# Optimization experiments

Hardware: AMD Instinct MI355X
Metric: run time of the kernel (lower is better)

## Reference

```python
import jax, jax.numpy as jnp
import numpy as np

EPS = 1e-5
CHUNK = 256
N_LAYERS = 4
D_MODEL = 1024
D_INNER = 2048
D_HEAD = 64
N_HEADS = 32
D_STATE = 64
D_CONV = 4
CONV_DIM = D_INNER + 2 * D_STATE  # ngroups=1
D_IN_PROJ = 2 * D_INNER + 2 * D_STATE + N_HEADS


def silu(x):
    return x * jax.nn.sigmoid(x)


def rmsnorm(x, w):
    return x * jax.lax.rsqrt(jnp.mean(x * x, axis=-1, keepdims=True) + EPS) * w


def segsum(x):
    # x: [..., T] -> [..., T, T] lower-triangular segment sums, -inf above diag
    T = x.shape[-1]
    cs = jnp.cumsum(x, axis=-1)
    ss = cs[..., :, None] - cs[..., None, :]
    mask = jnp.tril(jnp.ones((T, T), dtype=bool))
    return jnp.where(mask, ss, -jnp.inf)


def ssd(X, A, B, C, chunk):
    # X: [b,l,h,p] (already scaled by dt), A: [b,l,h] (= dt * A_head), B,C: [b,l,n] (ngroups=1)
    b, l, h, p = X.shape
    c = l // chunk
    X = X.reshape(b, c, chunk, h, p)
    A = A.reshape(b, c, chunk, h).transpose(0, 3, 1, 2)  # [b,h,c,l]
    B = B.reshape(b, c, chunk, -1)
    C = C.reshape(b, c, chunk, -1)
    Acs = jnp.cumsum(A, axis=-1)  # [b,h,c,l]
    # intra-chunk (diagonal blocks)
    Lm = jnp.exp(segsum(A))  # [b,h,c,l,l]
    Y_diag = jnp.einsum('bcln,bcsn,bhcls,bcshp->bclhp', C, B, Lm, X)
    # chunk end states
    decay_states = jnp.exp(Acs[..., -1:] - Acs)  # [b,h,c,l]
    states = jnp.einsum('bcln,bhcl,bclhp->bchpn', B, decay_states, X)
    # inter-chunk recurrence (c is small -> dense segsum over chunks)
    A_last = jnp.pad(Acs[..., -1], ((0, 0), (0, 0), (1, 0)))  # [b,h,c+1]
    decay_chunk = jnp.exp(segsum(A_last))  # [b,h,c+1,c+1]
    states = jnp.concatenate([jnp.zeros_like(states[:, :1]), states], axis=1)
    new_states = jnp.einsum('bhzc,bchpn->bzhpn', decay_chunk, states)
    states = new_states[:, :-1]  # state entering each chunk
    Y_off = jnp.einsum('bcln,bchpn,bhcl->bclhp', C, states, jnp.exp(Acs))
    return (Y_diag + Y_off).reshape(b, l, h, p)


def mamba2_layer(x, in_w, conv_w, conv_b, dt_bias, A_log, D, gnorm_w, out_w):
    b, l, _ = x.shape
    zxbcdt = jnp.einsum('bld,ed->ble', x, in_w)  # [b,l,D_IN_PROJ]
    z = zxbcdt[..., :D_INNER]
    xBC = zxbcdt[..., D_INNER:D_INNER + CONV_DIM]
    dt = zxbcdt[..., D_INNER + CONV_DIM:]  # [b,l,h]
    # depthwise causal conv1d + silu
    xpad = jnp.pad(xBC, ((0, 0), (D_CONV - 1, 0), (0, 0)))
    xconv = conv_b
    for k in range(D_CONV):
        xconv = xconv + xpad[:, k:k + l, :] * conv_w[:, k]
    xBC = silu(xconv)
    x_in = xBC[..., :D_INNER]
    B = xBC[..., D_INNER:D_INNER + D_STATE]
    C = xBC[..., D_INNER + D_STATE:]
    dt = jax.nn.softplus(dt + dt_bias)  # [b,l,h]
    A = -jnp.exp(A_log)  # [h]
    X = x_in.reshape(b, l, N_HEADS, D_HEAD)
    y = ssd(X * dt[..., None], dt * A, B, C, CHUNK)
    y = y + D[None, None, :, None] * X
    y = y.reshape(b, l, D_INNER)
    y = rmsnorm(y * silu(z), gnorm_w)
    return jnp.einsum('ble,de->bld', y, out_w)


def setup_inputs() -> dict:
    key = jax.random.key(0)
    ks = jax.random.split(key, 8)
    x = jax.random.normal(ks[0], (2, 2048, D_MODEL), dtype=jnp.float32)
    in_proj_w = jax.random.normal(ks[1], (N_LAYERS, D_IN_PROJ, D_MODEL), dtype=jnp.float32) * 0.02
    conv_w = jax.random.uniform(ks[2], (N_LAYERS, CONV_DIM, D_CONV), dtype=jnp.float32, minval=-0.5, maxval=0.5)
    conv_b = jnp.zeros((N_LAYERS, CONV_DIM), dtype=jnp.float32)
    A_log = jnp.log(jax.random.uniform(ks[3], (N_LAYERS, N_HEADS), dtype=jnp.float32, minval=1.0, maxval=16.0))
    dt0 = jax.random.uniform(ks[4], (N_LAYERS, N_HEADS), dtype=jnp.float32, minval=0.001, maxval=0.1)
    dt_bias = dt0 + jnp.log(-jnp.expm1(-dt0))  # inverse softplus
    D = jnp.ones((N_LAYERS, N_HEADS), dtype=jnp.float32)
    gnorm_w = jnp.ones((N_LAYERS, D_INNER), dtype=jnp.float32)
    out_proj_w = jax.random.normal(ks[5], (N_LAYERS, D_MODEL, D_INNER), dtype=jnp.float32) * 0.02
    rms_w = jnp.ones((N_LAYERS, D_MODEL), dtype=jnp.float32)
    return {"x": x, "in_proj_w": in_proj_w, "conv_w": conv_w, "conv_b": conv_b,
            "dt_bias": dt_bias, "A_log": A_log, "D": D, "gnorm_w": gnorm_w,
            "out_proj_w": out_proj_w, "rms_w": rms_w}


def reference(x, in_proj_w, conv_w, conv_b, dt_bias, A_log, D, gnorm_w, out_proj_w, rms_w):
    for i in range(N_LAYERS):
        x = x + mamba2_layer(rmsnorm(x, rms_w[i]), in_proj_w[i], conv_w[i], conv_b[i],
                             dt_bias[i], A_log[i], D[i], gnorm_w[i], out_proj_w[i])
    return x
```

## Files before the change

kernel.cpp:

```cpp
#include <hip/hip_runtime.h>
#include <cmath>

#define BATCH 2
#define LSEQ 2048
#define DMODEL 1024
#define DINNER 2048
#define NHEADS 32
#define DHEAD 64
#define DSTATE 64
#define DCONV 4
#define CONVDIM (DINNER + 2*DSTATE)
#define DINPROJ (2*DINNER + 2*DSTATE + NHEADS)
#define DINPROJ_PAD 4352
#define CHUNKSZ 256
#define NCHUNK (LSEQ/CHUNKSZ)
#define MROWS (BATCH*LSEQ)
#define EPSF 1e-5f

typedef __attribute__((ext_vector_type(8))) short shortx8;
typedef __attribute__((ext_vector_type(4))) short shortx4;
typedef __attribute__((ext_vector_type(4))) float floatx4;

__device__ __forceinline__ ushort f2bf(float f) {
  unsigned u = __float_as_uint(f);
  unsigned r = (u + 0x7fffu + ((u >> 16) & 1u)) >> 16;
  return (ushort)r;
}
__device__ __forceinline__ float bf2f(ushort b) {
  return __uint_as_float(((unsigned)b) << 16);
}

__device__ __forceinline__ shortx8 pack8(float4 a, float4 b) {
  shortx8 r;
  r[0] = (short)f2bf(a.x); r[1] = (short)f2bf(a.y);
  r[2] = (short)f2bf(a.z); r[3] = (short)f2bf(a.w);
  r[4] = (short)f2bf(b.x); r[5] = (short)f2bf(b.y);
  r[6] = (short)f2bf(b.z); r[7] = (short)f2bf(b.w);
  return r;
}

__device__ __forceinline__ void async_load16(const void* g, void* l) {
  __builtin_amdgcn_global_load_lds(
      (const __attribute__((address_space(1))) void*)g,
      (__attribute__((address_space(3))) void*)l, 16, 0, 0);
}

__device__ __forceinline__ float block_reduce_sum_256(float v, float* sb) {
  for (int off = 32; off > 0; off >>= 1) v += __shfl_down(v, off, 64);
  int lane = threadIdx.x & 63, wid = threadIdx.x >> 6;
  if (lane == 0) sb[wid] = v;
  __syncthreads();
  return sb[0] + sb[1] + sb[2] + sb[3];
}

__global__ __launch_bounds__(256) void cvt_bf16_k(const float* __restrict__ src,
                                                  ushort* __restrict__ dst,
                                                  size_t n_src, size_t n_dst) {
  size_t i = (size_t)blockIdx.x * 256 + threadIdx.x;
  if (i >= n_dst) return;
  float v = (i < n_src) ? src[i] : 0.f;
  dst[i] = f2bf(v);
}

__global__ __launch_bounds__(256) void cvt_w_all(const float* __restrict__ in_w,
                                                 const float* __restrict__ out_w,
                                                 ushort* __restrict__ in_bf,
                                                 ushort* __restrict__ out_bf) {
  unsigned g = (blockIdx.x * 256u + threadIdx.x) * 8u;
  const unsigned PL = (unsigned)DINPROJ_PAD * DMODEL;
  const unsigned n1 = 4u * PL;
  const unsigned n2 = 4u * DMODEL * DINNER;
  if (g < n1) {
    unsigned layer = g / PL, rem = g % PL;
    unsigned row = rem / DMODEL, col = rem % DMODEL;
    shortx8 o;
    if (row < DINPROJ) {
      const float* sp = in_w + ((size_t)layer * DINPROJ + row) * DMODEL + col;
      float4 a = *(const float4*)sp;
      float4 b = *(const float4*)(sp + 4);
      o = pack8(a, b);
    } else {
#pragma unroll
      for (int j = 0; j < 8; j++) o[j] = 0;
    }
    *(shortx8*)(in_bf + g) = o;
  } else if (g < n1 + n2) {
    unsigned j = g - n1;
    const float* sp = out_w + j;
    float4 a = *(const float4*)sp;
    float4 b = *(const float4*)(sp + 4);
    *(shortx8*)(out_bf + j) = pack8(a, b);
  }
}

__global__ __launch_bounds__(256) void rmsnorm_k(const float* __restrict__ x,
                                                 const float* __restrict__ w,
                                                 ushort* __restrict__ out) {
  __shared__ float sb[4];
  int r = blockIdx.x;
  const float* xr = x + (size_t)r * DMODEL;
  ushort* orow = out + (size_t)r * DMODEL;
  int c0 = threadIdx.x * 4;
  float4 v4 = *(const float4*)(xr + c0);
  float ssq = v4.x * v4.x + v4.y * v4.y + v4.z * v4.z + v4.w * v4.w;
  float s = block_reduce_sum_256(ssq, sb);
  float sc = rsqrtf(s / (float)DMODEL + EPSF);
  float4 w4 = *(const float4*)(w + c0);
  shortx4 o;
  o[0] = (short)f2bf(v4.x * sc * w4.x);
  o[1] = (short)f2bf(v4.y * sc * w4.y);
  o[2] = (short)f2bf(v4.z * sc * w4.z);
  o[3] = (short)f2bf(v4.w * sc * w4.w);
  *(shortx4*)(orow + c0) = o;
}

__device__ __forceinline__ void stage_tile(const ushort* __restrict__ A,
                                           const ushort* __restrict__ B,
                                           char* lb, int m0, int n0, int K, int k0,
                                           int wid, int rA, int sA) {
#pragma unroll
  for (int rd = 0; rd < 2; rd++) {
    int r = rd * 64 + rA;
    int sl = sA ^ ((r ^ (r >> 2)) & 3);
    async_load16(A + (size_t)(m0 + r) * K + (k0 + sl * 8), lb + rd * 4096 + wid * 1024);
  }
#pragma unroll
  for (int rd = 0; rd < 2; rd++) {
    int r = rd * 64 + rA;
    int sl = sA ^ ((r ^ (r >> 2)) & 3);
    async_load16(B + (size_t)(n0 + r) * K + (k0 + sl * 8), lb + 8192 + rd * 4096 + wid * 1024);
  }
}

__global__ __launch_bounds__(256, 3) void gemm_nt_mfma_pipe(
    const ushort* __restrict__ A, const ushort* __restrict__ B,
    ushort* __restrict__ Cbf, int M, int N, int K,
    int nbx, int rw, int rh) {
  __shared__ __align__(16) char lds[3][16384];
  int tid = threadIdx.x;
  int wid = tid >> 6, lane = tid & 63;
  int quad = lane >> 4, lrow = lane & 15;

  int d = blockIdx.x;
  int xcd = d & 7, wi = d >> 3;
  int ra = nbx / rw;
  int rn = xcd % ra, rm = xcd / ra;
  int bx = rn * rw + wi % rw;
  int by = rm * rh + wi / rw;

  int m0 = by * 128, n0 = bx * 128;
  int wm = (wid >> 1) * 64, wn = (wid & 1) * 64;
  int rA = tid >> 2, sA = tid & 3;

  floatx4 acc[4][4];
#pragma unroll
  for (int i = 0; i < 4; i++)
#pragma unroll
    for (int j = 0; j < 4; j++) acc[i][j] = (floatx4){0.f, 0.f, 0.f, 0.f};

  int NT = K >> 5;
#pragma unroll
  for (int t = 0; t < 2; t++)
    stage_tile(A, B, lds[t], m0, n0, K, t * 32, wid, rA, sA);

  int cur = 0, sb = 2;
  for (int t = 0; t < NT; t++) {
    if (t < NT - 1) asm volatile("s_waitcnt vmcnt(4)" ::: "memory");
    else            asm volatile("s_waitcnt vmcnt(0)" ::: "memory");
    __builtin_amdgcn_s_barrier();
    __builtin_amdgcn_sched_barrier(0);
    if (t + 2 < NT) {
      stage_tile(A, B, lds[sb], m0, n0, K, (t + 2) * 32, wid, rA, sA);
      sb = (sb == 2) ? 0 : sb + 1;
    }

    const char* Ab = lds[cur];
    const char* Bb = Ab + 8192;
    cur = (cur == 2) ? 0 : cur + 1;
    shortx8 af[4], bfr[4];
#pragma unroll
    for (int i = 0; i < 4; i++) {
      int r = wm + i * 16 + lrow;
      af[i] = *(const shortx8*)(Ab + r * 64 + ((quad ^ ((r ^ (r >> 2)) & 3)) << 4));
    }
#pragma unroll
    for (int j = 0; j < 4; j++) {
      int r = wn + j * 16 + lrow;
      bfr[j] = *(const shortx8*)(Bb + r * 64 + ((quad ^ ((r ^ (r >> 2)) & 3)) << 4));
    }
    __builtin_amdgcn_s_setprio(1);
#pragma unroll
    for (int i = 0; i < 4; i++)
#pragma unroll
      for (int j = 0; j < 4; j++)
        acc[i][j] = __builtin_amdgcn_mfma_f32_16x16x32_bf16(af[i], bfr[j], acc[i][j], 0, 0, 0);
    __builtin_amdgcn_s_setprio(0);
  }

#pragma unroll
  for (int i = 0; i < 4; i++) {
    int r0 = m0 + wm + i * 16 + quad * 4;
#pragma unroll
    for (int j = 0; j < 4; j++) {
      int n = n0 + wn + j * 16 + lrow;
      if (n < N)
#pragma unroll
        for (int r = 0; r < 4; r++)
          Cbf[(size_t)(r0 + r) * N + n] = f2bf(acc[i][j][r]);
    }
  }
}

__device__ __forceinline__ void stage_tile64(const ushort* __restrict__ A,
                                             const ushort* __restrict__ B,
                                             char* lb, int m0, int n0, int K, int k0,
                                             int wid, int rA, int sA) {
#pragma unroll
  for (int rd = 0; rd < 2; rd++) {
    int r = rd * 64 + rA;
    int sl = sA ^ ((r ^ (r >> 2)) & 3);
    async_load16(A + (size_t)(m0 + r) * K + (k0 + sl * 8), lb + rd * 4096 + wid * 1024);
  }
  {
    int r = rA;
    int sl = sA ^ ((r ^ (r >> 2)) & 3);
    async_load16(B + (size_t)(n0 + r) * K + (k0 + sl * 8), lb + 8192 + wid * 1024);
  }
}

__global__ __launch_bounds__(256, 2) void gemm_nt_64(
    const ushort* __restrict__ A, const ushort* __restrict__ B,
    float* __restrict__ C, const float* __restrict__ resid,
    int M, int N, int K, int nbx, int rw, int rh) {
  __shared__ __align__(16) char lds[3][12288];
  int tid = threadIdx.x;
  int wid = tid >> 6, lane = tid & 63;
  int quad = lane >> 4, lrow = lane & 15;

  int d = blockIdx.x;
  int xcd = d & 7, wi = d >> 3;
  int ra = nbx / rw;
  int rn = xcd % ra, rm = xcd / ra;
  int bx = rn * rw + wi % rw;
  int by = rm * rh + wi / rw;

  int m0 = by * 128, n0 = bx * 64;
  int wm = (wid >> 1) * 64, wn = (wid & 1) * 32;
  int rA = tid >> 2, sA = tid & 3;

  floatx4 acc[4][2];
#pragma unroll
  for (int i = 0; i < 4; i++)
#pragma unroll
    for (int j = 0; j < 2; j++) acc[i][j] = (floatx4){0.f, 0.f, 0.f, 0.f};

  int NT = K >> 5;
#pragma unroll
  for (int t = 0; t < 2; t++)
    stage_tile64(A, B, lds[t], m0, n0, K, t * 32, wid, rA, sA);

  int cur = 0, sb = 2;
  for (int t = 0; t < NT; t++) {
    if (t < NT - 1) asm volatile("s_waitcnt vmcnt(3)" ::: "memory");
    else            asm volatile("s_waitcnt vmcnt(0)" ::: "memory");
    __builtin_amdgcn_s_barrier();
    __builtin_amdgcn_sched_barrier(0);
    if (t + 2 < NT) {
      stage_tile64(A, B, lds[sb], m0, n0, K, (t + 2) * 32, wid, rA, sA);
      sb = (sb == 2) ? 0 : sb + 1;
    }

    const char* Ab = lds[cur];
    const char* Bb = Ab + 8192;
    cur = (cur == 2) ? 0 : cur + 1;
    shortx8 af[4], bfr[2];
#pragma unroll
    for (int i = 0; i < 4; i++) {
      int r = wm + i * 16 + lrow;
      af[i] = *(const shortx8*)(Ab + r * 64 + ((quad ^ ((r ^ (r >> 2)) & 3)) << 4));
    }
#pragma unroll
    for (int j = 0; j < 2; j++) {
      int r = wn + j * 16 + lrow;
      bfr[j] = *(const shortx8*)(Bb + r * 64 + ((quad ^ ((r ^ (r >> 2)) & 3)) << 4));
    }
    __builtin_amdgcn_s_setprio(1);
#pragma unroll
    for (int i = 0; i < 4; i++)
#pragma unroll
      for (int j = 0; j < 2; j++)
        acc[i][j] = __builtin_amdgcn_mfma_f32_16x16x32_bf16(af[i], bfr[j], acc[i][j], 0, 0, 0);
    __builtin_amdgcn_s_setprio(0);
  }

  bool hasR = (resid != nullptr);
#pragma unroll
  for (int i = 0; i < 4; i++) {
    int r0 = m0 + wm + i * 16 + quad * 4;
#pragma unroll
    for (int j = 0; j < 2; j++) {
      int n = n0 + wn + j * 16 + lrow;
#pragma unroll
      for (int r = 0; r < 4; r++) {
        size_t idx = (size_t)(r0 + r) * N + n;
        float v = acc[i][j][r];
        if (hasR) v += resid[idx];
        C[idx] = v;
      }
    }
  }
}

__global__ __launch_bounds__(256) void convcum_k(const ushort* __restrict__ zxbf,
                                                 const float* __restrict__ cw,
                                                 const float* __restrict__ cb,
                                                 ushort* __restrict__ xbf,
                                                 const float* __restrict__ dt_bias,
                                                 const float* __restrict__ A_log,
                                                 float* __restrict__ dt_sp,
                                                 float* __restrict__ dtA_cs) {
  __shared__ float buf[256];
  int tid = threadIdx.x;
  if (blockIdx.x < MROWS / 8) {
    int r0 = blockIdx.x * 8;
    int bstart = r0 & ~(LSEQ - 1);
#pragma unroll
    for (int rep = 0; rep < 2; rep++) {
      int ch;
      if (rep == 0) ch = tid * 8;
      else { if (tid >= (CONVDIM - 2048) / 8) break; ch = 2048 + tid * 8; }
      float wv[8][4], bias[8];
#pragma unroll
      for (int j = 0; j < 8; j++) {
        float4 w4 = *(const float4*)(cw + (ch + j) * 4);
        wv[j][0] = w4.x; wv[j][1] = w4.y; wv[j][2] = w4.z; wv[j][3] = w4.w;
        bias[j] = cb[ch + j];
      }
      float xw[11][8];
#pragma unroll
      for (int wr = 0; wr < 11; wr++) {
        int rr = r0 - 3 + wr;
        if (rr < bstart) {
#pragma unroll
          for (int j = 0; j < 8; j++) xw[wr][j] = 0.f;
        } else {
          shortx8 v = *(const shortx8*)(zxbf + (size_t)rr * DINPROJ + DINNER + ch);
#pragma unroll
          for (int j = 0; j < 8; j++) xw[wr][j] = bf2f((ushort)v[j]);
        }
      }
#pragma unroll
      for (int o = 0; o < 8; o++) {
        shortx8 ov;
#pragma unroll
        for (int j = 0; j < 8; j++) {
          float acc = bias[j];
#pragma unroll
          for (int k = 0; k < 4; k++) acc += xw[o + k][j] * wv[j][k];
          float s = acc / (1.f + expf(-acc));
          ov[j] = (short)f2bf(s);
        }
        *(shortx8*)(xbf + (size_t)(r0 + o) * CONVDIM + ch) = ov;
      }
    }
  } else {
    int bid = blockIdx.x - MROWS / 8;
    int h = bid & 31, c = (bid >> 5) & 7, b = bid >> 8;
    int l = tid;
    float Aneg = -expf(A_log[h]);
    int row = b * LSEQ + c * CHUNKSZ + l;
    float v = bf2f(zxbf[(size_t)row * DINPROJ + DINNER + CONVDIM + h]) + dt_bias[h];
    float dtv = (v > 20.f) ? v : log1pf(expf(v));
    dt_sp[row * 32 + h] = dtv;
    buf[l] = dtv * Aneg;
    __syncthreads();
    for (int off = 1; off < 256; off <<= 1) {
      float add = (l >= off) ? buf[l - off] : 0.f;
      __syncthreads();
      buf[l] += add;
      __syncthreads();
    }
    dtA_cs[(size_t)bid * CHUNKSZ + l] = buf[l];
  }
}

#define ST_STRIDE 72
__global__ __launch_bounds__(256) void states_mfma(const ushort* __restrict__ xbf,
                                                   const float* __restrict__ dt_sp,
                                                   const float* __restrict__ dtA_cs,
                                                   float* __restrict__ st_raw) {
  __shared__ ushort XT[64 * ST_STRIDE];
  __shared__ ushort BT[64 * ST_STRIDE];
  __shared__ float wrow[64];
  int bid = blockIdx.x;
  int h = bid & 31, c = (bid >> 5) & 7, b = bid >> 8;
  int tid = threadIdx.x;
  int w = tid >> 6, lane = tid & 63;
  int quad = lane >> 4, lrow = lane & 15;
  int cbase = bid * CHUNKSZ;
  int rowbase = b * LSEQ + c * CHUNKSZ;
  float T = dtA_cs[cbase + CHUNKSZ - 1];
  floatx4 acc[4];
  for (int jt = 0; jt < 4; jt++) acc[jt] = (floatx4){0.f, 0.f, 0.f, 0.f};
  int half = tid & 31, srb = tid >> 5;
  int ekey = (half & 7) << 3;
  for (int lt = 0; lt < 4; lt++) {
    __syncthreads();
    if (tid < 64) {
      int row = rowbase + lt * 64 + tid;
      wrow[tid] = dt_sp[row * 32 + h] * __expf(T - dtA_cs[cbase + lt * 64 + tid]);
    }
    __syncthreads();
    for (int pass = 0; pass < 8; pass++) {
      int sr = srb + pass * 8;
      int row = rowbase + lt * 64 + sr;
      uint bv = *(const uint*)(xbf + (size_t)row * CONVDIM + DINNER + 2 * half);
      uint xv = *(const uint*)(xbf + (size_t)row * CONVDIM + h * DHEAD + 2 * half);
      float wv = wrow[sr];
      int sc = sr ^ ekey;
      BT[(2 * half) * ST_STRIDE + sc]     = (ushort)(bv & 0xffff);
      BT[(2 * half + 1) * ST_STRIDE + sc] = (ushort)(bv >> 16);
      XT[(2 * half) * ST_STRIDE + sc]     = f2bf(bf2f((ushort)(xv & 0xffff)) * wv);
      XT[(2 * half + 1) * ST_STRIDE + sc] = f2bf(bf2f((ushort)(xv >> 16)) * wv);
    }
    __syncthreads();
    int arow = w * 16 + lrow;
    int akey = ((arow >> 1) & 7) << 3;
    for (int kk = 0; kk < 64; kk += 32) {
      shortx8 af = *(const shortx8*)&XT[arow * ST_STRIDE + ((kk + quad * 8) ^ akey)];
      for (int jt = 0; jt < 4; jt++) {
        int brow = jt * 16 + lrow;
        int bkey = ((brow >> 1) & 7) << 3;
        shortx8 bf = *(const shortx8*)&BT[brow * ST_STRIDE + ((kk + quad * 8) ^ bkey)];
        acc[jt] = __builtin_amdgcn_mfma_f32_16x16x32_bf16(af, bf, acc[jt], 0, 0, 0);
      }
    }
  }
  size_t base = (size_t)bid * (DHEAD * DSTATE);
  for (int jt = 0; jt < 4; jt++) {
    int n = jt * 16 + lrow;
    for (int r = 0; r < 4; r++) {
      int p = w * 16 + quad * 4 + r;
      st_raw[base + (size_t)p * 64 + n] = acc[jt][r];
    }
  }
}

__global__ __launch_bounds__(256) void scan_k(float* __restrict__ st,
                                              const float* __restrict__ dtA_cs) {
  int bid = blockIdx.x;
  int seg = bid & 3, h = (bid >> 2) & 31, b = bid >> 7;
  int tid = threadIdx.x;
  int off = seg * 1024;
  float s[4];
  for (int i = 0; i < 4; i++) s[i] = 0.f;
  for (int c = 0; c < NCHUNK; c++) {
    int g = (b * NCHUNK + c) * 32 + h;
    float dec = expf(dtA_cs[(size_t)g * CHUNKSZ + CHUNKSZ - 1]);
    size_t base = (size_t)g * (DHEAD * DSTATE) + off;
    for (int i = 0; i < 4; i++) {
      int idx = tid + i * 256;
      float raw = st[base + idx];
      st[base + idx] = s[i];
      s[i] = s[i] * dec + raw;
    }
  }
}

#define BS_STRIDE 72
#define XT_STRIDE 68
#define PW_STRIDE 72
__global__ __launch_bounds__(256) void ydiag_mfma(const ushort* __restrict__ xbf,
                                                  const float* __restrict__ dt_sp,
                                                  const float* __restrict__ dtA_cs,
                                                  const float* __restrict__ st_in,
                                                  ushort* __restrict__ Y) {
  __shared__ ushort Bs[64 * BS_STRIDE];
  __shared__ ushort XsT[64 * XT_STRIDE];
  __shared__ ushort Pw[4 * 16 * PW_STRIDE];
  __shared__ float cs[256];
  int tid = threadIdx.x;
  int w = tid >> 6, lane = tid & 63;
  int quad = lane >> 4, lrow = lane & 15;
  int bid = blockIdx.x;
  int lt = bid & 3, h = (bid >> 2) & 31, c = (bid >> 7) & 7, b = bid >> 10;
  int g = (b * NCHUNK + c) * 32 + h;
  int cbase = g * CHUNKSZ;
  int rowbase = b * LSEQ + c * CHUNKSZ;

  cs[tid] = dtA_cs[cbase + tid];
  __syncthreads();

  int mrow = lt * 64 + w * 16;
  float csl[4];
  for (int r = 0; r < 4; r++) csl[r] = cs[mrow + quad * 4 + r];

  shortx8 Cf[2];
  {
    const ushort* cp = xbf + (size_t)(rowbase + mrow + lrow) * CONVDIM + DINNER + DSTATE;
    for (int q = 0; q < 2; q++)
      Cf[q] = *(const shortx8*)(cp + q * 32 + quad * 8);
  }

  floatx4 acc[4];
  for (int jt = 0; jt < 4; jt++) acc[jt] = (floatx4){0.f, 0.f, 0.f, 0.f};
  const float* stp = st_in + (size_t)g * (DHEAD * DSTATE);
  for (int q = 0; q < 2; q++) {
    for (int jt = 0; jt < 4; jt++) {
      const float* sp = stp + (size_t)(jt * 16 + lrow) * 64 + q * 32 + quad * 8;
      shortx8 sf = pack8(*(const float4*)sp, *(const float4*)(sp + 4));
      acc[jt] = __builtin_amdgcn_mfma_f32_16x16x32_bf16(Cf[q], sf, acc[jt], 0, 0, 0);
    }
  }
  for (int jt = 0; jt < 4; jt++)
    for (int r = 0; r < 4; r++) acc[jt][r] *= __expf(csl[r]);

  ushort* myP = Pw + w * 16 * PW_STRIDE;
  int half = tid & 31, srb = tid >> 5;
  for (int st = 0; st <= lt; st++) {
    __syncthreads();
    for (int pass = 0; pass < 8; pass++) {
      int sr = srb + pass * 8;
      int row = rowbase + st * 64 + sr;
      uint bv = *(const uint*)(xbf + (size_t)row * CONVDIM + DINNER + 2 * half);
      *(uint*)&Bs[sr * BS_STRIDE + 2 * half] = bv;
      float dtv = dt_sp[row * 32 + h];
      uint xv = *(const uint*)(xbf + (size_t)row * CONVDIM + h * DHEAD + 2 * half);
      XsT[(2 * half) * XT_STRIDE + sr]     = f2bf(bf2f((ushort)(xv & 0xffff)) * dtv);
      XsT[(2 * half + 1) * XT_STRIDE + sr] = f2bf(bf2f((ushort)(xv >> 16)) * dtv);
    }
    __syncthreads();
    for (int jt = 0; jt < 4; jt++) {
      floatx4 s = (floatx4){0.f, 0.f, 0.f, 0.f};
      for (int q = 0; q < 2; q++) {
        shortx8 bfr = *(const shortx8*)&Bs[(jt * 16 + lrow) * BS_STRIDE + q * 32 + quad * 8];
        s = __builtin_amdgcn_mfma_f32_16x16x32_bf16(Cf[q], bfr, s, 0, 0, 0);
      }
      int scol = st * 64 + jt * 16 + lrow;
      float css = cs[scol];
      for (int r = 0; r < 4; r++) {
        int l = mrow + quad * 4 + r;
        float v = (scol <= l) ? s[r] * __expf(csl[r] - css) : 0.f;
        myP[(quad * 4 + r) * PW_STRIDE + jt * 16 + lrow] = f2bf(v);
      }
    }
    shortx8 pf[2];
    for (int q = 0; q < 2; q++)
      pf[q] = *(const shortx8*)&myP[lrow * PW_STRIDE + q * 32 + quad * 8];
    for (int jt = 0; jt < 4; jt++) {
      for (int q = 0; q < 2; q++) {
        const ushort* xp = &XsT[(jt * 16 + lrow) * XT_STRIDE + q * 32 + quad * 8];
        shortx4 lo = *(const shortx4*)xp;
        shortx4 hi = *(const shortx4*)(xp + 4);
        shortx8 xf = __builtin_shufflevector(lo, hi, 0, 1, 2, 3, 4, 5, 6, 7);
        acc[jt] = __builtin_amdgcn_mfma_f32_16x16x32_bf16(pf[q], xf, acc[jt], 0, 0, 0);
      }
    }
  }
  int growb = rowbase + mrow + quad * 4;
  for (int jt = 0; jt < 4; jt++)
    for (int r = 0; r < 4; r++)
      Y[(size_t)(growb + r) * DINNER + h * DHEAD + jt * 16 + lrow] = f2bf(acc[jt][r]);
}

__global__ __launch_bounds__(256) void gatenorm_k(const ushort* __restrict__ Ybf,
                                                  const ushort* __restrict__ zxbf,
                                                  const ushort* __restrict__ xbf,
                                                  const float* __restrict__ Dvec,
                                                  const float* __restrict__ gw,
                                                  ushort* __restrict__ obf) {
  __shared__ float sb[4];
  int r = blockIdx.x;
  int c0 = threadIdx.x * 8;
  const ushort* yr = Ybf + (size_t)r * DINNER;
  const ushort* zr = zxbf + (size_t)r * DINPROJ;
  const ushort* xr = xbf + (size_t)r * CONVDIM;
  ushort* orow = obf + (size_t)r * DINNER;
  shortx8 y8 = *(const shortx8*)(yr + c0);
  shortx8 z8 = *(const shortx8*)(zr + c0);
  shortx8 x8 = *(const shortx8*)(xr + c0);
  float Dv = Dvec[threadIdx.x >> 3];
  float t[8]; float ssq = 0.f;
#pragma unroll
  for (int i = 0; i < 8; i++) {
    float z = bf2f((ushort)z8[i]);
    float yv = bf2f((ushort)y8[i]) + Dv * bf2f((ushort)x8[i]);
    float gv = yv * (z / (1.f + expf(-z)));
    t[i] = gv;
    ssq += gv * gv;
  }
  float s = block_reduce_sum_256(ssq, sb);
  float sc = rsqrtf(s / (float)DINNER + EPSF);
  float4 g0 = *(const float4*)(gw + c0);
  float4 g1 = *(const float4*)(gw + c0 + 4);
  shortx8 o;
  o[0] = (short)f2bf(t[0] * sc * g0.x); o[1] = (short)f2bf(t[1] * sc * g0.y);
  o[2] = (short)f2bf(t[2] * sc * g0.z); o[3] = (short)f2bf(t[3] * sc * g0.w);
  o[4] = (short)f2bf(t[4] * sc * g1.x); o[5] = (short)f2bf(t[5] * sc * g1.y);
  o[6] = (short)f2bf(t[6] * sc * g1.z); o[7] = (short)f2bf(t[7] * sc * g1.w);
  *(shortx8*)(orow + c0) = o;
}

extern "C" void kernel_launch(void* const* d_in, const int* in_sizes, int n_in,
                              void* d_out, int out_size, void* d_ws, size_t ws_size,
                              hipStream_t stream) {
  const float* x_in     = (const float*)d_in[0];
  const float* in_w     = (const float*)d_in[1];
  const float* conv_w   = (const float*)d_in[2];
  const float* conv_b   = (const float*)d_in[3];
  const float* dt_bias  = (const float*)d_in[4];
  const float* A_log    = (const float*)d_in[5];
  const float* Dvec     = (const float*)d_in[6];
  const float* gnorm_w  = (const float*)d_in[7];
  const float* out_w    = (const float*)d_in[8];
  const float* rms_w    = (const float*)d_in[9];
  float* out = (float*)d_out;

  float* ws = (float*)d_ws;
  size_t o = 0;
  float* x_cur  = ws + o; o += (size_t)MROWS * DMODEL;
  ushort* zx_bf = (ushort*)(ws + o); o += (size_t)MROWS * DINPROJ / 2;
  ushort* xbf   = (ushort*)(ws + o); o += (size_t)MROWS * CONVDIM / 2;
  float* dt_sp  = ws + o; o += (size_t)MROWS * NHEADS;
  float* dtA_cs = ws + o; o += (size_t)BATCH * NCHUNK * NHEADS * CHUNKSZ;
  float* st     = ws + o; o += (size_t)BATCH * NCHUNK * NHEADS * DHEAD * DSTATE;
  ushort* Ybf   = (ushort*)(ws + o); o += (size_t)MROWS * DINNER / 2;
  ushort* act_bf = (ushort*)(ws + o); o += (size_t)MROWS * DINNER / 2;
  size_t base_f = o;

  size_t inw_f  = (size_t)4 * DINPROJ_PAD * DMODEL / 2;
  size_t outw_f = (size_t)4 * DMODEL * DINNER / 2;
  bool hoist = ws_size >= (base_f + inw_f + outw_f) * sizeof(float);

  ushort* in_bf_all = (ushort*)(ws + base_f);
  ushort* out_bf_all = (ushort*)(ws + base_f + inw_f);
  ushort* w_bf_fb = (ushort*)(ws + base_f);

  hipMemcpyAsync(x_cur, x_in, (size_t)MROWS * DMODEL * sizeof(float),
                 hipMemcpyDeviceToDevice, stream);

  if (hoist) {
    unsigned ntot = (4u * DINPROJ_PAD * DMODEL + 4u * DMODEL * DINNER) / 8u;
    cvt_w_all<<<(ntot + 255) / 256, 256, 0, stream>>>(in_w, out_w, in_bf_all, out_bf_all);
  }

  for (int i = 0; i < 4; i++) {
    const float* conv_w_i = conv_w  + (size_t)i * CONVDIM * DCONV;
    const float* conv_b_i = conv_b  + (size_t)i * CONVDIM;
    const float* dtb_i    = dt_bias + (size_t)i * NHEADS;
    const float* Alog_i   = A_log   + (size_t)i * NHEADS;
    const float* D_i      = Dvec    + (size_t)i * NHEADS;
    const float* gw_i     = gnorm_w + (size_t)i * DINNER;
    const float* rms_w_i  = rms_w   + (size_t)i * DMODEL;

    const ushort* w1_bf;
    const ushort* w2_bf;
    if (hoist) {
      w1_bf = in_bf_all  + (size_t)i * DINPROJ_PAD * DMODEL;
      w2_bf = out_bf_all + (size_t)i * DMODEL * DINNER;
    } else {
      size_t ns = (size_t)DINPROJ * DMODEL, nd = (size_t)DINPROJ_PAD * DMODEL;
      cvt_bf16_k<<<(nd + 255) / 256, 256, 0, stream>>>(
          in_w + (size_t)i * DINPROJ * DMODEL, w_bf_fb, ns, nd);
      w1_bf = w_bf_fb;
      w2_bf = w_bf_fb;
    }

    rmsnorm_k<<<MROWS, 256, 0, stream>>>(x_cur, rms_w_i, act_bf);
    gemm_nt_mfma_pipe<<<(DINPROJ_PAD / 128) * (MROWS / 128), 256, 0, stream>>>(
        act_bf, w1_bf, zx_bf, MROWS, DINPROJ, DMODEL, DINPROJ_PAD / 128, 17, 8);
    convcum_k<<<MROWS / 8 + BATCH * NCHUNK * NHEADS, 256, 0, stream>>>(
        zx_bf, conv_w_i, conv_b_i, xbf, dtb_i, Alog_i, dt_sp, dtA_cs);
    states_mfma<<<BATCH * NCHUNK * NHEADS, 256, 0, stream>>>(xbf, dt_sp, dtA_cs, st);
    scan_k<<<BATCH * NHEADS * 4, 256, 0, stream>>>(st, dtA_cs);
    ydiag_mfma<<<BATCH * NCHUNK * NHEADS * 4, 256, 0, stream>>>(
        xbf, dt_sp, dtA_cs, st, Ybf);
    gatenorm_k<<<MROWS, 256, 0, stream>>>(Ybf, zx_bf, xbf, D_i, gw_i, act_bf);
    if (!hoist) {
      size_t ns = (size_t)DMODEL * DINNER;
      cvt_bf16_k<<<(ns + 255) / 256, 256, 0, stream>>>(
          out_w + (size_t)i * DMODEL * DINNER, (ushort*)w_bf_fb, ns, ns);
    }
    float* outC = (i == 3) ? out : x_cur;
    gemm_nt_64<<<(MROWS / 128) * (DMODEL / 64), 256, 0, stream>>>(
        act_bf, w2_bf, outC, x_cur, MROWS, DMODEL, DINNER, DMODEL / 64, 8, 8);
  }
}
```

Baseline: 887.4 us.

## Shrink out-proj GEMM tile to 64x64 and vectorize SSD global loads

The out-projection GEMM tile drops from 128x64 to 64x64. This doubles the grid, lowers LDS use, and raises the occupancy hint to 4 blocks per CU. Separately, the states and ydiag kernels now load each row's B and X with 16-byte vector loads instead of many 4-byte loads, then scatter them into the transposed LDS tiles. The smaller tile gives more parallelism on the 4096x1024 output but less operand reuse per block, and the scattered LDS writes may cause bank conflicts.

```diff
diff --git a/kernel.cpp b/kernel.cpp
--- a/kernel.cpp
+++ b/kernel.cpp
@@ -215,24 +215,16 @@
                                              const ushort* __restrict__ B,
                                              char* lb, int m0, int n0, int K, int k0,
                                              int wid, int rA, int sA) {
-#pragma unroll
-  for (int rd = 0; rd < 2; rd++) {
-    int r = rd * 64 + rA;
-    int sl = sA ^ ((r ^ (r >> 2)) & 3);
-    async_load16(A + (size_t)(m0 + r) * K + (k0 + sl * 8), lb + rd * 4096 + wid * 1024);
-  }
-  {
-    int r = rA;
-    int sl = sA ^ ((r ^ (r >> 2)) & 3);
-    async_load16(B + (size_t)(n0 + r) * K + (k0 + sl * 8), lb + 8192 + wid * 1024);
-  }
-}
-
-__global__ __launch_bounds__(256, 2) void gemm_nt_64(
+  int sl = sA ^ ((rA ^ (rA >> 2)) & 3);
+  async_load16(A + (size_t)(m0 + rA) * K + (k0 + sl * 8), lb + wid * 1024);
+  async_load16(B + (size_t)(n0 + rA) * K + (k0 + sl * 8), lb + 4096 + wid * 1024);
+}
+
+__global__ __launch_bounds__(256, 4) void gemm_nt_64(
     const ushort* __restrict__ A, const ushort* __restrict__ B,
     float* __restrict__ C, const float* __restrict__ resid,
     int M, int N, int K, int nbx, int rw, int rh) {
-  __shared__ __align__(16) char lds[3][12288];
+  __shared__ __align__(16) char lds[3][8192];
   int tid = threadIdx.x;
   int wid = tid >> 6, lane = tid & 63;
   int quad = lane >> 4, lrow = lane & 15;
@@ -244,13 +236,13 @@
   int bx = rn * rw + wi % rw;
   int by = rm * rh + wi / rw;
 
-  int m0 = by * 128, n0 = bx * 64;
-  int wm = (wid >> 1) * 64, wn = (wid & 1) * 32;
+  int m0 = by * 64, n0 = bx * 64;
+  int wm = (wid >> 1) * 32, wn = (wid & 1) * 32;
   int rA = tid >> 2, sA = tid & 3;
 
-  floatx4 acc[4][2];
-#pragma unroll
-  for (int i = 0; i < 4; i++)
+  floatx4 acc[2][2];
+#pragma unroll
+  for (int i = 0; i < 2; i++)
 #pragma unroll
     for (int j = 0; j < 2; j++) acc[i][j] = (floatx4){0.f, 0.f, 0.f, 0.f};
 
@@ -261,7 +253,7 @@
 
   int cur = 0, sb = 2;
   for (int t = 0; t < NT; t++) {
-    if (t < NT - 1) asm volatile("s_waitcnt vmcnt(3)" ::: "memory");
+    if (t < NT - 1) asm volatile("s_waitcnt vmcnt(2)" ::: "memory");
     else            asm volatile("s_waitcnt vmcnt(0)" ::: "memory");
     __builtin_amdgcn_s_barrier();
     __builtin_amdgcn_sched_barrier(0);
@@ -271,11 +263,11 @@
     }
 
     const char* Ab = lds[cur];
-    const char* Bb = Ab + 8192;
+    const char* Bb = Ab + 4096;
     cur = (cur == 2) ? 0 : cur + 1;
-    shortx8 af[4], bfr[2];
-#pragma unroll
-    for (int i = 0; i < 4; i++) {
+    shortx8 af[2], bfr[2];
+#pragma unroll
+    for (int i = 0; i < 2; i++) {
       int r = wm + i * 16 + lrow;
       af[i] = *(const shortx8*)(Ab + r * 64 + ((quad ^ ((r ^ (r >> 2)) & 3)) << 4));
     }
@@ -286,7 +278,7 @@
     }
     __builtin_amdgcn_s_setprio(1);
 #pragma unroll
-    for (int i = 0; i < 4; i++)
+    for (int i = 0; i < 2; i++)
 #pragma unroll
       for (int j = 0; j < 2; j++)
         acc[i][j] = __builtin_amdgcn_mfma_f32_16x16x32_bf16(af[i], bfr[j], acc[i][j], 0, 0, 0);
@@ -295,7 +287,7 @@
 
   bool hasR = (resid != nullptr);
 #pragma unroll
-  for (int i = 0; i < 4; i++) {
+  for (int i = 0; i < 2; i++) {
     int r0 = m0 + wm + i * 16 + quad * 4;
 #pragma unroll
     for (int j = 0; j < 2; j++) {
@@ -402,8 +394,7 @@
   float T = dtA_cs[cbase + CHUNKSZ - 1];
   floatx4 acc[4];
   for (int jt = 0; jt < 4; jt++) acc[jt] = (floatx4){0.f, 0.f, 0.f, 0.f};
-  int half = tid & 31, srb = tid >> 5;
-  int ekey = (half & 7) << 3;
+  int row_l = tid >> 2, seg = tid & 3;
   for (int lt = 0; lt < 4; lt++) {
     __syncthreads();
     if (tid < 64) {
@@ -411,17 +402,26 @@
       wrow[tid] = dt_sp[row * 32 + h] * __expf(T - dtA_cs[cbase + lt * 64 + tid]);
     }
     __syncthreads();
-    for (int pass = 0; pass < 8; pass++) {
-      int sr = srb + pass * 8;
-      int row = rowbase + lt * 64 + sr;
-      uint bv = *(const uint*)(xbf + (size_t)row * CONVDIM + DINNER + 2 * half);
-      uint xv = *(const uint*)(xbf + (size_t)row * CONVDIM + h * DHEAD + 2 * half);
-      float wv = wrow[sr];
-      int sc = sr ^ ekey;
-      BT[(2 * half) * ST_STRIDE + sc]     = (ushort)(bv & 0xffff);
-      BT[(2 * half + 1) * ST_STRIDE + sc] = (ushort)(bv >> 16);
-      XT[(2 * half) * ST_STRIDE + sc]     = f2bf(bf2f((ushort)(xv & 0xffff)) * wv);
-      XT[(2 * half + 1) * ST_STRIDE + sc] = f2bf(bf2f((ushort)(xv >> 16)) * wv);
+    {
+      int row = rowbase + lt * 64 + row_l;
+      const ushort* bp = xbf + (size_t)row * CONVDIM + DINNER + seg * 16;
+      const ushort* xp = xbf + (size_t)row * CONVDIM + h * DHEAD + seg * 16;
+      shortx8 b0 = *(const shortx8*)bp;
+      shortx8 b1 = *(const shortx8*)(bp + 8);
+      shortx8 x0 = *(const shortx8*)xp;
+      shortx8 x1 = *(const shortx8*)(xp + 8);
+      float wv = wrow[row_l];
+#pragma unroll
+      for (int j = 0; j < 8; j++) {
+        int c0 = seg * 16 + j;
+        int c1 = c0 + 8;
+        int k0 = ((c0 >> 1) & 7) << 3;
+        int k1 = ((c1 >> 1) & 7) << 3;
+        BT[c0 * ST_STRIDE + (row_l ^ k0)] = (ushort)b0[j];
+        BT[c1 * ST_STRIDE + (row_l ^ k1)] = (ushort)b1[j];
+        XT[c0 * ST_STRIDE + (row_l ^ k0)] = f2bf(bf2f((ushort)x0[j]) * wv);
+        XT[c1 * ST_STRIDE + (row_l ^ k1)] = f2bf(bf2f((ushort)x1[j]) * wv);
+      }
     }
     __syncthreads();
     int arow = w * 16 + lrow;
@@ -516,18 +516,26 @@
     for (int r = 0; r < 4; r++) acc[jt][r] *= __expf(csl[r]);
 
   ushort* myP = Pw + w * 16 * PW_STRIDE;
-  int half = tid & 31, srb = tid >> 5;
+  int row_l = tid >> 2, seg = tid & 3;
   for (int st = 0; st <= lt; st++) {
     __syncthreads();
-    for (int pass = 0; pass < 8; pass++) {
-      int sr = srb + pass * 8;
-      int row = rowbase + st * 64 + sr;
-      uint bv = *(const uint*)(xbf + (size_t)row * CONVDIM + DINNER + 2 * half);
-      *(uint*)&Bs[sr * BS_STRIDE + 2 * half] = bv;
+    {
+      int row = rowbase + st * 64 + row_l;
+      const ushort* bp = xbf + (size_t)row * CONVDIM + DINNER + seg * 16;
+      const ushort* xp = xbf + (size_t)row * CONVDIM + h * DHEAD + seg * 16;
+      shortx8 b0 = *(const shortx8*)bp;
+      shortx8 b1 = *(const shortx8*)(bp + 8);
+      shortx8 x0 = *(const shortx8*)xp;
+      shortx8 x1 = *(const shortx8*)(xp + 8);
       float dtv = dt_sp[row * 32 + h];
-      uint xv = *(const uint*)(xbf + (size_t)row * CONVDIM + h * DHEAD + 2 * half);
-      XsT[(2 * half) * XT_STRIDE + sr]     = f2bf(bf2f((ushort)(xv & 0xffff)) * dtv);
-      XsT[(2 * half + 1) * XT_STRIDE + sr] = f2bf(bf2f((ushort)(xv >> 16)) * dtv);
+      *(shortx8*)&Bs[row_l * BS_STRIDE + seg * 16] = b0;
+      *(shortx8*)&Bs[row_l * BS_STRIDE + seg * 16 + 8] = b1;
+#pragma unroll
+      for (int j = 0; j < 8; j++) {
+        int c0 = seg * 16 + j;
+        XsT[c0 * XT_STRIDE + row_l]       = f2bf(bf2f((ushort)x0[j]) * dtv);
+        XsT[(c0 + 8) * XT_STRIDE + row_l] = f2bf(bf2f((ushort)x1[j]) * dtv);
+      }
     }
     __syncthreads();
     for (int jt = 0; jt < 4; jt++) {
@@ -682,7 +690,7 @@
           out_w + (size_t)i * DMODEL * DINNER, (ushort*)w_bf_fb, ns, ns);
     }
     float* outC = (i == 3) ? out : x_cur;
-    gemm_nt_64<<<(MROWS / 128) * (DMODEL / 64), 256, 0, stream>>>(
-        act_bf, w2_bf, outC, x_cur, MROWS, DMODEL, DINNER, DMODEL / 64, 8, 8);
-  }
-}
+    gemm_nt_64<<<(MROWS / 64) * (DMODEL / 64), 256, 0, stream>>>(
+        act_bf, w2_bf, outC, x_cur, MROWS, DMODEL, DINNER, DMODEL / 64, 8, 16);
+  }
+}
```

New measurement: 904.9 us. About the same (+2.0%).
